# Performance work log

Hardware: AMD Instinct MI355X
Metric: run time of the kernel (lower is better)

## Reference

```python
import jax, jax.numpy as jnp
import numpy as np

V = 100000      # voca_size
EMB = 128       # embedding_size
REG = 7         # region_size
NC = 20         # num_classes
ML = 512        # max_length
B = 64          # batch
RAD = REG // 2
ENT = ML - 2 * RAD


def setup_inputs() -> dict:
    key = jax.random.key(0)
    k0, k1, k2, k3, k4, k5, k6 = jax.random.split(key, 7)
    train_input = jax.random.randint(k0, (B, ML), 0, V, dtype=jnp.int32)
    # embedding tables, uniform(-0.01, 0.01), padding row 0 zeroed (padding_idx=0)
    W_region = jax.random.uniform(k1, (V, REG * EMB), jnp.float32, -0.01, 0.01).at[0].set(0.0)
    W_word = jax.random.uniform(k2, (V, EMB), jnp.float32, -0.01, 0.01).at[0].set(0.0)
    # linear layers stored as [in, out]; xavier-uniform-like init
    lim1 = float(np.sqrt(6.0 / (EMB + 2 * ML)))
    W1 = jax.random.uniform(k3, (EMB, 2 * ML), jnp.float32, -lim1, lim1)
    b1 = jax.random.uniform(k4, (2 * ML,), jnp.float32, -0.01, 0.01)
    lim2 = float(np.sqrt(6.0 / (2 * ML + NC)))
    W2 = jax.random.uniform(k5, (2 * ML, NC), jnp.float32, -lim2, lim2)
    b2 = jax.random.uniform(k6, (NC,), jnp.float32, -0.01, 0.01)
    return {"train_input": train_input, "W_region": W_region, "W_word": W_word,
            "W1": W1, "b1": b1, "W2": W2, "b2": b2}


def reference(train_input, W_region, W_word, W1, b1, W2, b2):
    Bn, L = train_input.shape
    ent = L - 2 * RAD
    # region embedding of trimmed sequence -> [B, ent, REG, EMB]
    trimmed = train_input[:, RAD:L - RAD]
    K = W_region[trimmed].reshape(Bn, ent, REG, EMB)
    # sliding windows: [B, ent, REG] gather (replaces the python cat loop)
    idx = jnp.arange(ent)[:, None] + jnp.arange(REG)[None, :]
    win = train_input[:, idx]                    # [B, ent, REG]
    win = jnp.transpose(win, (0, 2, 1))          # [B, REG, ent] (matches torch transposes)
    E = W_word[win]                              # [B, REG, ent, EMB]
    # faithful to torch: a reshape (not transpose) back to [B, ent, REG, EMB]
    E = E.reshape(Bn, ent, REG, EMB)
    # max over region dim, sum over sequence dim -> [B, EMB]
    noi = jnp.sum(jnp.max(E * K, axis=2), axis=1)
    # small MLP (dropout is identity in eval mode)
    h = jax.nn.relu(noi @ W1 + b1)
    logits = h @ W2 + b2
    prob = jax.nn.softmax(logits, axis=1)
    cls = jnp.argmax(prob, axis=1)
    return logits, prob, cls
```

## Files before the change

kernel.cpp:

```cpp
#include <hip/hip_runtime.h>
#include <hip/hip_bf16.h>

#define V    100000
#define EMB  128
#define REG  7
#define NC   20
#define ML   512
#define BB   64
#define RAD  3
#define ENT  506
#define TI   32
#define NBLK 16

__global__ __launch_bounds__(256) void noi_partial_kernel(
    const int*   __restrict__ train,
    const float* __restrict__ Wr,
    const float* __restrict__ Ww,
    float*       __restrict__ partial)
{
    __shared__ int   idx_lds[TI * 8];
    __shared__ float red[4][EMB];

    const int blk = blockIdx.x;
    const int b   = blk >> 4;
    const int i0  = (blk & 15) * TI;
    const int tid = threadIdx.x;

    {
        const int il  = tid >> 3;
        const int sub = tid & 7;
        const int i   = i0 + il;
        int v = 0;
        if (i < ENT) {
            if (sub == 0) {
                v = train[b * ML + i + RAD];
            } else {
                const int t = i * REG + (sub - 1);
                const int r = t / ENT;
                const int e = t - r * ENT;
                v = train[b * ML + e + r];
            }
        }
        idx_lds[tid] = v;
    }
    __syncthreads();

    const int w    = tid >> 6;
    const int lane = tid & 63;

    float accx = 0.f, accy = 0.f;
    for (int il = w; il < TI; il += 4) {
        const int i = i0 + il;
        if (i >= ENT) break;
        const int base = il * 8;
        const int ridx = idx_lds[base];
        const float2* Krow = (const float2*)(Wr + (size_t)ridx * (REG * EMB));

        float mx, my;
        {
            const float2* Erow = (const float2*)(Ww + (size_t)idx_lds[base + 1] * EMB);
            const float2 k = Krow[lane];
            const float2 e = Erow[lane];
            mx = k.x * e.x;
            my = k.y * e.y;
        }
        #pragma unroll
        for (int j = 1; j < REG; ++j) {
            const float2* Erow = (const float2*)(Ww + (size_t)idx_lds[base + 1 + j] * EMB);
            const float2 k = Krow[j * 64 + lane];
            const float2 e = Erow[lane];
            mx = fmaxf(mx, k.x * e.x);
            my = fmaxf(my, k.y * e.y);
        }
        accx += mx;
        accy += my;
    }

    red[w][2 * lane]     = accx;
    red[w][2 * lane + 1] = accy;
    __syncthreads();
    if (tid < EMB) {
        const float s = red[0][tid] + red[1][tid] + red[2][tid] + red[3][tid];
        partial[(size_t)blk * EMB + tid] = s;
    }
}

__global__ __launch_bounds__(256) void mlp_kernel(
    const float* __restrict__ partial,
    const float* __restrict__ W1,
    const float* __restrict__ b1,
    const float* __restrict__ W2,
    const float* __restrict__ b2,
    float*       __restrict__ out)
{
    __shared__ float noi[EMB];
    __shared__ float h[2 * ML];
    __shared__ float lg[NC];

    const int b   = blockIdx.x;
    const int tid = threadIdx.x;

    if (tid < EMB) {
        float s = 0.f;
        #pragma unroll
        for (int k = 0; k < NBLK; ++k)
            s += partial[(size_t)(b * NBLK + k) * EMB + tid];
        noi[tid] = s;
    }
    __syncthreads();

    float h0 = b1[tid], h1 = b1[tid + 256], h2 = b1[tid + 512], h3 = b1[tid + 768];
    for (int k = 0; k < EMB; ++k) {
        const float nk = noi[k];
        const float* row = W1 + k * (2 * ML);
        h0 = fmaf(nk, row[tid],       h0);
        h1 = fmaf(nk, row[tid + 256], h1);
        h2 = fmaf(nk, row[tid + 512], h2);
        h3 = fmaf(nk, row[tid + 768], h3);
    }
    h[tid]       = fmaxf(h0, 0.f);
    h[tid + 256] = fmaxf(h1, 0.f);
    h[tid + 512] = fmaxf(h2, 0.f);
    h[tid + 768] = fmaxf(h3, 0.f);
    __syncthreads();

    const int w    = tid >> 6;
    const int lane = tid & 63;
    for (int c = w; c < NC; c += 4) {
        float p = 0.f;
        #pragma unroll 4
        for (int k = lane; k < 2 * ML; k += 64)
            p = fmaf(h[k], W2[k * NC + c], p);
        for (int off = 32; off; off >>= 1)
            p += __shfl_down(p, off);
        if (lane == 0) lg[c] = p + b2[c];
    }
    __syncthreads();

    if (tid == 0) {
        float mx = lg[0];
        for (int c = 1; c < NC; ++c) mx = fmaxf(mx, lg[c]);
        float pr[NC];
        float s = 0.f;
        for (int c = 0; c < NC; ++c) { pr[c] = expf(lg[c] - mx); s += pr[c]; }
        const float inv = 1.f / s;
        int am = 0; float best = lg[0];
        for (int c = 1; c < NC; ++c) if (lg[c] > best) { best = lg[c]; am = c; }
        for (int c = 0; c < NC; ++c) {
            out[b * NC + c]           = lg[c];
            out[BB * NC + b * NC + c] = pr[c] * inv;
        }
        out[2 * BB * NC + b] = (float)am;
    }
}

extern "C" void kernel_launch(void* const* d_in, const int* in_sizes, int n_in,
                              void* d_out, int out_size, void* d_ws, size_t ws_size,
                              hipStream_t stream) {
    const int*   train = (const int*)  d_in[0];
    const float* Wr    = (const float*)d_in[1];
    const float* Ww    = (const float*)d_in[2];
    const float* W1    = (const float*)d_in[3];
    const float* b1    = (const float*)d_in[4];
    const float* W2    = (const float*)d_in[5];
    const float* b2    = (const float*)d_in[6];
    float* out     = (float*)d_out;
    float* partial = (float*)d_ws;

    hipLaunchKernelGGL(noi_partial_kernel, dim3(BB * NBLK), dim3(256), 0, stream,
                       train, Wr, Ww, partial);
    hipLaunchKernelGGL(mlp_kernel, dim3(BB), dim3(256), 0, stream,
                       partial, W1, b1, W2, b2, out);
}
```

Measured before the change: 468.6 us.

## Fuse gather and MLP kernels via last-block atomic counter and prefetch gathers

Merges the region-embedding reduction and the MLP into one kernel. The last block to finish for each batch row, detected with an atomic counter, runs the MLP and softmax. The gather loop is software-pipelined so the next row's seven K and E loads are issued before the current row is computed, which raises memory-level parallelism. It also swaps expf for __expf and adds a memset launch to reset the counters, which costs extra register pressure and a serialized tail per batch row.

```diff
diff --git a/kernel.cpp b/kernel.cpp
--- a/kernel.cpp
+++ b/kernel.cpp
@@ -12,14 +12,24 @@
 #define TI   32
 #define NBLK 16
 
-__global__ __launch_bounds__(256) void noi_partial_kernel(
+__global__ __launch_bounds__(256) void fused_kernel(
     const int*   __restrict__ train,
     const float* __restrict__ Wr,
     const float* __restrict__ Ww,
-    float*       __restrict__ partial)
+    const float* __restrict__ W1,
+    const float* __restrict__ b1,
+    const float* __restrict__ W2,
+    const float* __restrict__ b2,
+    float*       __restrict__ partial,
+    int*         __restrict__ ctr,
+    float*       __restrict__ out)
 {
     __shared__ int   idx_lds[TI * 8];
     __shared__ float red[4][EMB];
+    __shared__ int   is_last;
+    __shared__ float noi[EMB];
+    __shared__ float hbuf[2 * ML];
+    __shared__ float lg[NC];
 
     const int blk = blockIdx.x;
     const int b   = blk >> 4;
@@ -47,33 +57,47 @@
 
     const int w    = tid >> 6;
     const int lane = tid & 63;
+    const int lim  = (ENT - i0 < TI) ? (ENT - i0) : TI;
 
     float accx = 0.f, accy = 0.f;
-    for (int il = w; il < TI; il += 4) {
-        const int i = i0 + il;
-        if (i >= ENT) break;
-        const int base = il * 8;
-        const int ridx = idx_lds[base];
-        const float2* Krow = (const float2*)(Wr + (size_t)ridx * (REG * EMB));
-
-        float mx, my;
+    {
+        int il = w;
+        float2 kv[REG], ev[REG];
         {
-            const float2* Erow = (const float2*)(Ww + (size_t)idx_lds[base + 1] * EMB);
-            const float2 k = Krow[lane];
-            const float2 e = Erow[lane];
-            mx = k.x * e.x;
-            my = k.y * e.y;
+            const int base = il * 8;
+            const float2* Krow = (const float2*)(Wr + (size_t)idx_lds[base] * (REG * EMB));
+            #pragma unroll
+            for (int j = 0; j < REG; ++j) {
+                kv[j] = Krow[j * 64 + lane];
+                ev[j] = ((const float2*)(Ww + (size_t)idx_lds[base + 1 + j] * EMB))[lane];
+            }
         }
-        #pragma unroll
-        for (int j = 1; j < REG; ++j) {
-            const float2* Erow = (const float2*)(Ww + (size_t)idx_lds[base + 1 + j] * EMB);
-            const float2 k = Krow[j * 64 + lane];
-            const float2 e = Erow[lane];
-            mx = fmaxf(mx, k.x * e.x);
-            my = fmaxf(my, k.y * e.y);
+        while (true) {
+            const int iln  = (il + 4 < lim) ? (il + 4) : il;
+            float2 kn[REG], en[REG];
+            {
+                const int base = iln * 8;
+                const float2* Krow = (const float2*)(Wr + (size_t)idx_lds[base] * (REG * EMB));
+                #pragma unroll
+                for (int j = 0; j < REG; ++j) {
+                    kn[j] = Krow[j * 64 + lane];
+                    en[j] = ((const float2*)(Ww + (size_t)idx_lds[base + 1 + j] * EMB))[lane];
+                }
+            }
+            float mx = kv[0].x * ev[0].x;
+            float my = kv[0].y * ev[0].y;
+            #pragma unroll
+            for (int j = 1; j < REG; ++j) {
+                mx = fmaxf(mx, kv[j].x * ev[j].x);
+                my = fmaxf(my, kv[j].y * ev[j].y);
+            }
+            accx += mx;
+            accy += my;
+            if (il + 4 >= lim) break;
+            il += 4;
+            #pragma unroll
+            for (int j = 0; j < REG; ++j) { kv[j] = kn[j]; ev[j] = en[j]; }
         }
-        accx += mx;
-        accy += my;
     }
 
     red[w][2 * lane]     = accx;
@@ -83,22 +107,15 @@
         const float s = red[0][tid] + red[1][tid] + red[2][tid] + red[3][tid];
         partial[(size_t)blk * EMB + tid] = s;
     }
-}
-
-__global__ __launch_bounds__(256) void mlp_kernel(
-    const float* __restrict__ partial,
-    const float* __restrict__ W1,
-    const float* __restrict__ b1,
-    const float* __restrict__ W2,
-    const float* __restrict__ b2,
-    float*       __restrict__ out)
-{
-    __shared__ float noi[EMB];
-    __shared__ float h[2 * ML];
-    __shared__ float lg[NC];
-
-    const int b   = blockIdx.x;
-    const int tid = threadIdx.x;
+    __threadfence();
+    __syncthreads();
+    if (tid == 0) {
+        const int old = atomicAdd(&ctr[b], 1);
+        is_last = (old == NBLK - 1) ? 1 : 0;
+    }
+    __syncthreads();
+    if (!is_last) return;
+    __threadfence();
 
     if (tid < EMB) {
         float s = 0.f;
@@ -118,19 +135,17 @@
         h2 = fmaf(nk, row[tid + 512], h2);
         h3 = fmaf(nk, row[tid + 768], h3);
     }
-    h[tid]       = fmaxf(h0, 0.f);
-    h[tid + 256] = fmaxf(h1, 0.f);
-    h[tid + 512] = fmaxf(h2, 0.f);
-    h[tid + 768] = fmaxf(h3, 0.f);
+    hbuf[tid]       = fmaxf(h0, 0.f);
+    hbuf[tid + 256] = fmaxf(h1, 0.f);
+    hbuf[tid + 512] = fmaxf(h2, 0.f);
+    hbuf[tid + 768] = fmaxf(h3, 0.f);
     __syncthreads();
 
-    const int w    = tid >> 6;
-    const int lane = tid & 63;
     for (int c = w; c < NC; c += 4) {
         float p = 0.f;
         #pragma unroll 4
         for (int k = lane; k < 2 * ML; k += 64)
-            p = fmaf(h[k], W2[k * NC + c], p);
+            p = fmaf(hbuf[k], W2[k * NC + c], p);
         for (int off = 32; off; off >>= 1)
             p += __shfl_down(p, off);
         if (lane == 0) lg[c] = p + b2[c];
@@ -142,7 +157,7 @@
         for (int c = 1; c < NC; ++c) mx = fmaxf(mx, lg[c]);
         float pr[NC];
         float s = 0.f;
-        for (int c = 0; c < NC; ++c) { pr[c] = expf(lg[c] - mx); s += pr[c]; }
+        for (int c = 0; c < NC; ++c) { pr[c] = __expf(lg[c] - mx); s += pr[c]; }
         const float inv = 1.f / s;
         int am = 0; float best = lg[0];
         for (int c = 1; c < NC; ++c) if (lg[c] > best) { best = lg[c]; am = c; }
@@ -166,9 +181,10 @@
     const float* b2    = (const float*)d_in[6];
     float* out     = (float*)d_out;
     float* partial = (float*)d_ws;
+    int*   ctr     = (int*)((char*)d_ws + (size_t)BB * NBLK * EMB * sizeof(float));
 
-    hipLaunchKernelGGL(noi_partial_kernel, dim3(BB * NBLK), dim3(256), 0, stream,
-                       train, Wr, Ww, partial);
-    hipLaunchKernelGGL(mlp_kernel, dim3(BB), dim3(256), 0, stream,
-                       partial, W1, b1, W2, b2, out);
+    hipMemsetAsync(ctr, 0, BB * sizeof(int), stream);
+
+    hipLaunchKernelGGL(fused_kernel, dim3(BB * NBLK), dim3(256), 0, stream,
+                       train, Wr, Ww, W1, b1, W2, b2, partial, ctr, out);
 }
```

Result: slower. 675.4 us (+44.1%).

## One wave per sequence position with all gathers issued upfront

Applied to the files above, without the earlier changes.

Each block now covers 4 positions, one per wavefront, instead of looping 32 positions over 4 waves. Grid grows from 1024 to 127x64 blocks. Each wave loads its window indices directly from global memory, dropping the LDS index stage and one barrier. It then issues all 7 region-row loads and 7 word-row loads before computing, which raises memory-level parallelism for the random gathers. The cost is more partial sums (127 per batch) for the MLP kernel to reduce, more block launches, and a switch to the fast __expf in softmax.

```diff
diff --git a/kernel.cpp b/kernel.cpp
--- a/kernel.cpp
+++ b/kernel.cpp
@@ -9,79 +9,60 @@
 #define BB   64
 #define RAD  3
 #define ENT  506
-#define TI   32
-#define NBLK 16
+#define NB2  127
 
-__global__ __launch_bounds__(256) void noi_partial_kernel(
+__global__ __launch_bounds__(256, 4) void noi_kernel(
     const int*   __restrict__ train,
     const float* __restrict__ Wr,
     const float* __restrict__ Ww,
     float*       __restrict__ partial)
 {
-    __shared__ int   idx_lds[TI * 8];
     __shared__ float red[4][EMB];
 
-    const int blk = blockIdx.x;
-    const int b   = blk >> 4;
-    const int i0  = (blk & 15) * TI;
-    const int tid = threadIdx.x;
-
-    {
-        const int il  = tid >> 3;
-        const int sub = tid & 7;
-        const int i   = i0 + il;
-        int v = 0;
-        if (i < ENT) {
-            if (sub == 0) {
-                v = train[b * ML + i + RAD];
-            } else {
-                const int t = i * REG + (sub - 1);
-                const int r = t / ENT;
-                const int e = t - r * ENT;
-                v = train[b * ML + e + r];
-            }
-        }
-        idx_lds[tid] = v;
-    }
-    __syncthreads();
-
+    const int b    = blockIdx.y;
+    const int c4   = blockIdx.x;
+    const int tid  = threadIdx.x;
     const int w    = tid >> 6;
     const int lane = tid & 63;
+    const int i    = c4 * 4 + w;
 
-    float accx = 0.f, accy = 0.f;
-    for (int il = w; il < TI; il += 4) {
-        const int i = i0 + il;
-        if (i >= ENT) break;
-        const int base = il * 8;
-        const int ridx = idx_lds[base];
-        const float2* Krow = (const float2*)(Wr + (size_t)ridx * (REG * EMB));
+    float mx = 0.f, my = 0.f;
+    if (i < ENT) {
+        const int* trow = train + b * ML;
+        const int  ridx = trow[i + RAD];
+        int widx[REG];
+        #pragma unroll
+        for (int j = 0; j < REG; ++j) {
+            const int t = i * REG + j;
+            const int r = t / ENT;
+            const int e = t - r * ENT;
+            widx[j] = trow[e + r];
+        }
 
-        float mx, my;
-        {
-            const float2* Erow = (const float2*)(Ww + (size_t)idx_lds[base + 1] * EMB);
-            const float2 k = Krow[lane];
-            const float2 e = Erow[lane];
-            mx = k.x * e.x;
-            my = k.y * e.y;
-        }
+        const float2* Kp = (const float2*)(Wr + (size_t)ridx * (REG * EMB));
+        float2 kv[REG], ev[REG];
+        #pragma unroll
+        for (int j = 0; j < REG; ++j)
+            kv[j] = Kp[j * 64 + lane];
+        #pragma unroll
+        for (int j = 0; j < REG; ++j)
+            ev[j] = ((const float2*)(Ww + (size_t)widx[j] * EMB))[lane];
+
+        mx = kv[0].x * ev[0].x;
+        my = kv[0].y * ev[0].y;
         #pragma unroll
         for (int j = 1; j < REG; ++j) {
-            const float2* Erow = (const float2*)(Ww + (size_t)idx_lds[base + 1 + j] * EMB);
-            const float2 k = Krow[j * 64 + lane];
-            const float2 e = Erow[lane];
-            mx = fmaxf(mx, k.x * e.x);
-            my = fmaxf(my, k.y * e.y);
+            mx = fmaxf(mx, kv[j].x * ev[j].x);
+            my = fmaxf(my, kv[j].y * ev[j].y);
         }
-        accx += mx;
-        accy += my;
     }
 
-    red[w][2 * lane]     = accx;
-    red[w][2 * lane + 1] = accy;
+    red[w][2 * lane]     = mx;
+    red[w][2 * lane + 1] = my;
     __syncthreads();
     if (tid < EMB) {
         const float s = red[0][tid] + red[1][tid] + red[2][tid] + red[3][tid];
-        partial[(size_t)blk * EMB + tid] = s;
+        partial[((size_t)b * NB2 + c4) * EMB + tid] = s;
     }
 }
 
@@ -101,10 +82,11 @@
     const int tid = threadIdx.x;
 
     if (tid < EMB) {
+        const float* p = partial + (size_t)b * NB2 * EMB + tid;
         float s = 0.f;
-        #pragma unroll
-        for (int k = 0; k < NBLK; ++k)
-            s += partial[(size_t)(b * NBLK + k) * EMB + tid];
+        #pragma unroll 8
+        for (int k = 0; k < NB2; ++k)
+            s += p[(size_t)k * EMB];
         noi[tid] = s;
     }
     __syncthreads();
@@ -142,7 +124,7 @@
         for (int c = 1; c < NC; ++c) mx = fmaxf(mx, lg[c]);
         float pr[NC];
         float s = 0.f;
-        for (int c = 0; c < NC; ++c) { pr[c] = expf(lg[c] - mx); s += pr[c]; }
+        for (int c = 0; c < NC; ++c) { pr[c] = __expf(lg[c] - mx); s += pr[c]; }
         const float inv = 1.f / s;
         int am = 0; float best = lg[0];
         for (int c = 1; c < NC; ++c) if (lg[c] > best) { best = lg[c]; am = c; }
@@ -167,7 +149,7 @@
     float* out     = (float*)d_out;
     float* partial = (float*)d_ws;
 
-    hipLaunchKernelGGL(noi_partial_kernel, dim3(BB * NBLK), dim3(256), 0, stream,
+    hipLaunchKernelGGL(noi_kernel, dim3(NB2, BB), dim3(256), 0, stream,
                        train, Wr, Ww, partial);
     hipLaunchKernelGGL(mlp_kernel, dim3(BB), dim3(256), 0, stream,
                        partial, W1, b1, W2, b2, out);
```

New measurement: 472.0 us. About the same (+0.7%).
